# Optimization experiments

Measured on AMD Instinct MI355X. Metric: run time of the kernel, lower is better.

## Reference

```python
import jax, jax.numpy as jnp
import numpy as np

B, TK, N = 32, 2048, 1024  # batch, encoder steps, 2*hidden_dim


def setup_inputs() -> dict:
    key = jax.random.key(0)
    ks = jax.random.split(key, 12)
    s = 0.02
    return {
        "s_t_hat": jax.random.normal(ks[0], (B, N), jnp.float32),
        "h": jax.random.normal(ks[1], (B, TK, N), jnp.float32),
        "enc_padding_mask": jax.random.uniform(ks[2], (B, TK), jnp.float32),
        "coverage": jax.random.uniform(ks[3], (B, TK), jnp.float32),
        "q_h": jax.random.normal(ks[4], (B, TK, N), jnp.float32),
        "W_h": jax.random.normal(ks[5], (N, N), jnp.float32) * s,
        "W_q": jax.random.normal(ks[6], (N, N), jnp.float32) * s,
        "W_c": jax.random.normal(ks[7], (N,), jnp.float32) * s,   # Linear(1, N) weight, squeezed
        "W_d": jax.random.normal(ks[8], (N, N), jnp.float32) * s,  # decode_proj weight
        "b_d": jnp.zeros((N,), jnp.float32),                       # decode_proj bias
        "v_w": jax.random.normal(ks[9], (N,), jnp.float32) * s,    # v: Linear(N, 1) weight, squeezed
    }


def reference(s_t_hat, h, enc_padding_mask, coverage, q_h, W_h, W_q, W_c, W_d, b_d, v_w):
    # projections (Linear: y = x @ W.T)
    enc_feat = jnp.einsum("btn,mn->btm", h, W_h)            # [B,TK,N]
    q_feat = jnp.einsum("btn,mn->btm", q_h, W_q)            # [B,TK,N]
    dec_feat = s_t_hat @ W_d.T + b_d                         # [B,N]
    cov_feat = coverage[..., None] * W_c                     # [B,TK,N]
    att = jnp.tanh(enc_feat + dec_feat[:, None, :] + q_feat + cov_feat)
    scores = jnp.einsum("btn,n->bt", att, v_w)               # [B,TK]
    attn_ = jax.nn.softmax(scores, axis=1) * enc_padding_mask
    attn = attn_ / jnp.sum(attn_, axis=1, keepdims=True)     # renormalized
    c_t = jnp.einsum("bt,btn->bn", attn, h)                  # context vector
    coverage_out = coverage + attn
    return (c_t, attn, coverage_out)
```

## Files before the change

### kernel.cpp

```cpp
#include <hip/hip_runtime.h>
#include <stdint.h>

#define Bsz 32
#define TKs 2048
#define Nf  1024
#define Msz (Bsz*TKs)
#define KTOT 2048

typedef __bf16 bf16x8 __attribute__((ext_vector_type(8)));
typedef float  f32x4  __attribute__((ext_vector_type(4)));
typedef float  f32x16 __attribute__((ext_vector_type(16)));

__device__ __forceinline__ unsigned pack_bf2(float f0, float f1){
  unsigned u0 = __float_as_uint(f0) + 0x8000u;
  unsigned u1 = __float_as_uint(f1) + 0x8000u;
  return __builtin_amdgcn_perm(u1, u0, 0x07060302u);
}

__device__ __forceinline__ float fast_tanh(float x){
  float e = __expf(2.f * x);
  return 1.f - 2.f * __builtin_amdgcn_rcpf(e + 1.f);
}

__device__ __forceinline__ void async16(void* lds, const void* g){
  __builtin_amdgcn_global_load_lds(
      (const __attribute__((address_space(1))) unsigned int*)g,
      (__attribute__((address_space(3))) unsigned int*)lds,
      16, 0, 0);
}

__global__ __launch_bounds__(256) void pack_w_kernel(
    const float* __restrict__ Wh, const float* __restrict__ Wq,
    unsigned short* __restrict__ Wcat)
{
  int idx = (blockIdx.x * 256 + threadIdx.x) * 4;
  int m = idx >> 11;
  int k = idx & 2047;
  const float* src = (k < 1024) ? (Wh + m * 1024 + k) : (Wq + m * 1024 + (k - 1024));
  float4 v = *(const float4*)src;
  uint2 p;
  p.x = pack_bf2(v.x, v.y);
  p.y = pack_bf2(v.z, v.w);
  *(uint2*)(Wcat + idx) = p;
}

__global__ __launch_bounds__(256) void pack_a_kernel(
    const float* __restrict__ h, const float* __restrict__ q,
    unsigned short* __restrict__ Acat)
{
  size_t idx = ((size_t)blockIdx.x * 256 + threadIdx.x) * 8;
  size_t r = idx >> 11;
  int c = (int)(idx & 2047);
  const float* src = (c < 1024) ? (h + r * 1024 + c) : (q + r * 1024 + (c - 1024));
  float4 v0 = ((const float4*)src)[0];
  float4 v1 = ((const float4*)src)[1];
  uint4 p;
  p.x = pack_bf2(v0.x, v0.y); p.y = pack_bf2(v0.z, v0.w);
  p.z = pack_bf2(v1.x, v1.y); p.w = pack_bf2(v1.z, v1.w);
  *(uint4*)(Acat + idx) = p;
}

__global__ __launch_bounds__(256) void dec_kernel(
    const float* __restrict__ s_t, const float* __restrict__ Wd,
    const float* __restrict__ bd, float* __restrict__ dec)
{
  __shared__ float sv[1024];
  const int b = blockIdx.y;
  const int mbase = blockIdx.x * 64;
  for (int i = threadIdx.x; i < 1024; i += 256) sv[i] = s_t[b * 1024 + i];
  __syncthreads();
  const int wave = threadIdx.x >> 6, lane = threadIdx.x & 63;
  #pragma unroll 4
  for (int i = 0; i < 16; ++i){
    int m = mbase + wave * 16 + i;
    const float4* wr = (const float4*)(Wd + (size_t)m * 1024 + lane * 16);
    const float4* sr = (const float4*)(sv + lane * 16);
    float s = 0.f;
    #pragma unroll
    for (int j = 0; j < 4; ++j){
      float4 w = wr[j], x = sr[j];
      s += w.x * x.x + w.y * x.y + w.z * x.z + w.w * x.w;
    }
    #pragma unroll
    for (int d = 1; d < 64; d <<= 1) s += __shfl_xor(s, d);
    if (lane == 0) dec[b * 1024 + m] = s + bd[m];
  }
}

__global__ __launch_bounds__(256) void gemm_fused_fast(
    const unsigned short* __restrict__ Acat,
    const unsigned short* __restrict__ Wcat,
    const float* __restrict__ dec, const float* __restrict__ cov,
    const float* __restrict__ Wc, const float* __restrict__ vw,
    float* __restrict__ scoresP)
{
  __shared__ __align__(16) unsigned short As[128 * 32];
  __shared__ __align__(16) unsigned short Bs[128 * 32];
  __shared__ float ssum[2][128];
  __shared__ float covS[128];

  const int tid  = threadIdx.x;
  const int wave = tid >> 6, lane = tid & 63;
  const int wm = wave & 1, wn = wave >> 1;
  const int l31 = lane & 31, half = lane >> 5;

  const int p = blockIdx.x;
  const int ntile = (p >> 3) & 7;
  const int mtile = (p & 7) + ((p >> 6) << 3);
  const size_t growbase = (size_t)mtile * 128;

  if (tid < 128) covS[tid] = cov[growbase + tid];

  f32x16 acc[2][2];
  #pragma unroll
  for (int i = 0; i < 2; ++i)
    #pragma unroll
    for (int j = 0; j < 2; ++j)
      #pragma unroll
      for (int r = 0; r < 16; ++r) acc[i][j][r] = 0.f;

  const int s0 = wave * 128 + lane;
  const int s1 = s0 + 64;
  const int r0 = s0 >> 2, g0 = (s0 & 3) ^ ((r0 >> 1) & 3);
  const int r1 = s1 >> 2, g1 = (s1 & 3) ^ ((r1 >> 1) & 3);
  const unsigned short* pA0 = Acat + (size_t)(mtile * 128 + r0) * 2048 + g0 * 8;
  const unsigned short* pA1 = Acat + (size_t)(mtile * 128 + r1) * 2048 + g1 * 8;
  const unsigned short* pB0 = Wcat + (size_t)(ntile * 128 + r0) * 2048 + g0 * 8;
  const unsigned short* pB1 = Wcat + (size_t)(ntile * 128 + r1) * 2048 + g1 * 8;
  unsigned short* ldsA0 = &As[wave * 1024];
  unsigned short* ldsA1 = &As[wave * 1024 + 512];
  unsigned short* ldsB0 = &Bs[wave * 1024];
  unsigned short* ldsB1 = &Bs[wave * 1024 + 512];

  const bf16x8* a_rd[2][2];
  const bf16x8* b_rd[2][2];
  #pragma unroll
  for (int mi = 0; mi < 2; ++mi)
    #pragma unroll
    for (int ks = 0; ks < 2; ++ks){
      int row = wm * 64 + mi * 32 + l31;
      int g = ks * 2 + half;
      int pos = g ^ ((row >> 1) & 3);
      a_rd[mi][ks] = (const bf16x8*)&As[row * 32 + pos * 8];
    }
  #pragma unroll
  for (int ni = 0; ni < 2; ++ni)
    #pragma unroll
    for (int ks = 0; ks < 2; ++ks){
      int row = wn * 64 + ni * 32 + l31;
      int g = ks * 2 + half;
      int pos = g ^ ((row >> 1) & 3);
      b_rd[ni][ks] = (const bf16x8*)&Bs[row * 32 + pos * 8];
    }

  for (int kt = 0; kt < KTOT / 32; ++kt){
    async16(ldsA0, pA0);
    async16(ldsA1, pA1);
    async16(ldsB0, pB0);
    async16(ldsB1, pB1);
    pA0 += 32; pA1 += 32; pB0 += 32; pB1 += 32;
    __syncthreads();
    bf16x8 af[2][2], bg[2][2];
    #pragma unroll
    for (int i = 0; i < 2; ++i)
      #pragma unroll
      for (int ks = 0; ks < 2; ++ks){ af[i][ks] = *a_rd[i][ks]; bg[i][ks] = *b_rd[i][ks]; }
    #pragma unroll
    for (int ks = 0; ks < 2; ++ks)
      #pragma unroll
      for (int mi = 0; mi < 2; ++mi)
        #pragma unroll
        for (int ni = 0; ni < 2; ++ni)
          acc[mi][ni] = __builtin_amdgcn_mfma_f32_32x32x16_bf16(
              af[mi][ks], bg[ni][ks], acc[mi][ni], 0, 0, 0);
    __syncthreads();
  }

  const int brow = (mtile * 128) >> 11;
  const float* decb = dec + brow * 1024;
  float dv[2], wc2[2], vw2[2];
  #pragma unroll
  for (int ni = 0; ni < 2; ++ni){
    int col = ntile * 128 + wn * 64 + ni * 32 + l31;
    dv[ni]  = decb[col];
    wc2[ni] = Wc[col];
    vw2[ni] = vw[col];
  }
  #pragma unroll
  for (int mi = 0; mi < 2; ++mi){
    #pragma unroll
    for (int r = 0; r < 16; ++r){
      int rl = wm * 64 + mi * 32 + (r & 3) + 8 * (r >> 2) + 4 * half;
      float cv = covS[rl];
      float s = 0.f;
      #pragma unroll
      for (int ni = 0; ni < 2; ++ni){
        float x = acc[mi][ni][r] + dv[ni] + cv * wc2[ni];
        s += vw2[ni] * fast_tanh(x);
      }
      #pragma unroll
      for (int d = 1; d < 32; d <<= 1) s += __shfl_xor(s, d);
      if (l31 == 0) ssum[wn][rl] = s;
    }
  }
  __syncthreads();
  if (tid < 128)
    scoresP[(size_t)ntile * Msz + growbase + tid] = ssum[0][tid] + ssum[1][tid];
}

#define AST 40

__global__ __launch_bounds__(256) void gemm_fused_fb(
    const float* __restrict__ h, const float* __restrict__ q,
    const unsigned short* __restrict__ Wcat,
    const float* __restrict__ dec, const float* __restrict__ cov,
    const float* __restrict__ Wc, const float* __restrict__ vw,
    float* __restrict__ scoresP)
{
  __shared__ unsigned short As[128 * AST];
  __shared__ unsigned short Bs[128 * AST];
  __shared__ float ssum[2][128];

  const int tid  = threadIdx.x;
  const int wave = tid >> 6, lane = tid & 63;
  const int wm = wave & 1, wn = wave >> 1;
  const int quad = lane >> 4, low = lane & 15;
  const int ntile = blockIdx.x;
  const int mtile = blockIdx.y;

  f32x4 acc[4][4];
  #pragma unroll
  for (int i = 0; i < 4; ++i)
    #pragma unroll
    for (int j = 0; j < 4; ++j) acc[i][j] = (f32x4){0.f, 0.f, 0.f, 0.f};

  const int sr = tid >> 1;
  const int sh = (tid & 1) * 16;
  const size_t a_goff = ((size_t)(mtile * 128 + sr)) * 1024 + sh;
  const size_t b_goff = ((size_t)(ntile * 128 + sr)) * 2048 + sh;
  unsigned short* a_st = &As[sr * AST + sh];
  unsigned short* b_st = &Bs[sr * AST + sh];

  const bf16x8* a_rd[4];
  const bf16x8* b_rd[4];
  #pragma unroll
  for (int i = 0; i < 4; ++i){
    a_rd[i] = (const bf16x8*)&As[(wm * 64 + i * 16 + low) * AST + quad * 8];
    b_rd[i] = (const bf16x8*)&Bs[(wn * 64 + i * 16 + low) * AST + quad * 8];
  }

  for (int kt = 0; kt < KTOT / 32; ++kt){
    const int k0 = kt * 32;
    {
      const float* src = (k0 < 1024) ? (h + a_goff + k0) : (q + a_goff + (k0 - 1024));
      float4 v0 = ((const float4*)src)[0];
      float4 v1 = ((const float4*)src)[1];
      float4 v2 = ((const float4*)src)[2];
      float4 v3 = ((const float4*)src)[3];
      uint4 p0, p1;
      p0.x = pack_bf2(v0.x, v0.y); p0.y = pack_bf2(v0.z, v0.w);
      p0.z = pack_bf2(v1.x, v1.y); p0.w = pack_bf2(v1.z, v1.w);
      p1.x = pack_bf2(v2.x, v2.y); p1.y = pack_bf2(v2.z, v2.w);
      p1.z = pack_bf2(v3.x, v3.y); p1.w = pack_bf2(v3.z, v3.w);
      ((uint4*)a_st)[0] = p0;
      ((uint4*)a_st)[1] = p1;
    }
    {
      const uint4* src = (const uint4*)(Wcat + b_goff + k0);
      uint4 w0 = src[0];
      uint4 w1 = src[1];
      ((uint4*)b_st)[0] = w0;
      ((uint4*)b_st)[1] = w1;
    }
    __syncthreads();
    bf16x8 af[4], bg[4];
    #pragma unroll
    for (int i = 0; i < 4; ++i){ af[i] = *a_rd[i]; bg[i] = *b_rd[i]; }
    #pragma unroll
    for (int mi = 0; mi < 4; ++mi)
      #pragma unroll
      for (int ni = 0; ni < 4; ++ni)
        acc[mi][ni] = __builtin_amdgcn_mfma_f32_16x16x32_bf16(af[mi], bg[ni], acc[mi][ni], 0, 0, 0);
    __syncthreads();
  }

  const int brow = (mtile * 128) >> 11;
  const float* decb = dec + brow * 1024;
  const int colbase = ntile * 128 + wn * 64 + low;
  float dv[4], wc4[4], vw4[4];
  #pragma unroll
  for (int ni = 0; ni < 4; ++ni){
    int col = colbase + ni * 16;
    dv[ni]  = decb[col];
    wc4[ni] = Wc[col];
    vw4[ni] = vw[col];
  }
  const size_t growbase = (size_t)mtile * 128;
  const int rowloc0 = wm * 64 + quad * 4;
  #pragma unroll
  for (int mi = 0; mi < 4; ++mi){
    #pragma unroll
    for (int r = 0; r < 4; ++r){
      int rl = rowloc0 + mi * 16 + r;
      float cv = cov[growbase + rl];
      float s = 0.f;
      #pragma unroll
      for (int ni = 0; ni < 4; ++ni){
        float x = acc[mi][ni][r] + dv[ni] + cv * wc4[ni];
        s += vw4[ni] * fast_tanh(x);
      }
      #pragma unroll
      for (int d = 1; d < 16; d <<= 1) s += __shfl_xor(s, d);
      if (low == 0) ssum[wn][rl] = s;
    }
  }
  __syncthreads();
  if (tid < 128)
    scoresP[(size_t)ntile * Msz + growbase + tid] = ssum[0][tid] + ssum[1][tid];
}

__global__ __launch_bounds__(256) void softmax_kernel(
    const float* __restrict__ scoresP, const float* __restrict__ mask,
    const float* __restrict__ cov, float* __restrict__ attn_o,
    float* __restrict__ cov_o)
{
  const int b = blockIdx.x;
  const int tid = threadIdx.x;
  const int wave = tid >> 6, lane = tid & 63;
  __shared__ float redm[4], reds[4];
  float sc[8];
  float mx = -3.4e38f;
  #pragma unroll
  for (int j = 0; j < 8; ++j){
    int t = tid + j * 256;
    float s = 0.f;
    #pragma unroll
    for (int p = 0; p < 8; ++p) s += scoresP[(size_t)p * Msz + b * TKs + t];
    sc[j] = s;
    mx = fmaxf(mx, s);
  }
  #pragma unroll
  for (int d = 1; d < 64; d <<= 1) mx = fmaxf(mx, __shfl_xor(mx, d));
  if (lane == 0) redm[wave] = mx;
  __syncthreads();
  mx = fmaxf(fmaxf(redm[0], redm[1]), fmaxf(redm[2], redm[3]));
  float e[8]; float sum = 0.f;
  #pragma unroll
  for (int j = 0; j < 8; ++j){
    int t = tid + j * 256;
    float v = __expf(sc[j] - mx) * mask[b * TKs + t];
    e[j] = v; sum += v;
  }
  #pragma unroll
  for (int d = 1; d < 64; d <<= 1) sum += __shfl_xor(sum, d);
  if (lane == 0) reds[wave] = sum;
  __syncthreads();
  sum = reds[0] + reds[1] + reds[2] + reds[3];
  float inv = 1.f / sum;
  #pragma unroll
  for (int j = 0; j < 8; ++j){
    int t = tid + j * 256;
    float a = e[j] * inv;
    attn_o[b * TKs + t] = a;
    cov_o[b * TKs + t]  = cov[b * TKs + t] + a;
  }
}

__global__ __launch_bounds__(256) void ct_partial_bf(
    const unsigned short* __restrict__ Acat, const float* __restrict__ attn,
    float* __restrict__ P)
{
  const int b = blockIdx.y, tc = blockIdx.x;
  const int c4 = threadIdx.x * 4;
  float4 acc = {0.f, 0.f, 0.f, 0.f};
  const size_t rbase = (size_t)b * TKs + tc * 64;
  const float* ab = attn + b * TKs + tc * 64;
  #pragma unroll 4
  for (int tt = 0; tt < 64; ++tt){
    float a = ab[tt];
    uint2 v = *(const uint2*)(Acat + (rbase + tt) * 2048 + c4);
    acc.x += a * __uint_as_float(v.x << 16);
    acc.y += a * __uint_as_float(v.x & 0xffff0000u);
    acc.z += a * __uint_as_float(v.y << 16);
    acc.w += a * __uint_as_float(v.y & 0xffff0000u);
  }
  *(float4*)(P + ((size_t)(tc * Bsz + b)) * Nf + c4) = acc;
}

__global__ __launch_bounds__(256) void ct_partial(
    const float* __restrict__ h, const float* __restrict__ attn,
    float* __restrict__ P)
{
  const int b = blockIdx.y, tc = blockIdx.x;
  const int n4 = threadIdx.x * 4;
  float4 acc = {0.f, 0.f, 0.f, 0.f};
  const float* hb = h + ((size_t)b * TKs + tc * 64) * Nf;
  const float* ab = attn + b * TKs + tc * 64;
  #pragma unroll 4
  for (int tt = 0; tt < 64; ++tt){
    float a = ab[tt];
    float4 hv = *(const float4*)(hb + (size_t)tt * Nf + n4);
    acc.x += a * hv.x; acc.y += a * hv.y; acc.z += a * hv.z; acc.w += a * hv.w;
  }
  *(float4*)(P + ((size_t)(tc * Bsz + b)) * Nf + n4) = acc;
}

__global__ __launch_bounds__(256) void ct_reduce(
    const float* __restrict__ P, float* __restrict__ out)
{
  int bn = (blockIdx.x * 256 + threadIdx.x) * 4;
  float4 s = {0.f, 0.f, 0.f, 0.f};
  for (int j = 0; j < 32; ++j){
    float4 v = *(const float4*)(P + (size_t)j * (Bsz * Nf) + bn);
    s.x += v.x; s.y += v.y; s.z += v.z; s.w += v.w;
  }
  *(float4*)(out + bn) = s;
}

extern "C" void kernel_launch(void* const* d_in, const int* in_sizes, int n_in,
                              void* d_out, int out_size, void* d_ws, size_t ws_size,
                              hipStream_t stream) {
  const float* s_t  = (const float*)d_in[0];
  const float* h    = (const float*)d_in[1];
  const float* mask = (const float*)d_in[2];
  const float* cov  = (const float*)d_in[3];
  const float* qh   = (const float*)d_in[4];
  const float* Wh   = (const float*)d_in[5];
  const float* Wq   = (const float*)d_in[6];
  const float* Wc   = (const float*)d_in[7];
  const float* Wd   = (const float*)d_in[8];
  const float* bd   = (const float*)d_in[9];
  const float* vw   = (const float*)d_in[10];

  float* out    = (float*)d_out;
  float* c_t    = out;
  float* attn_o = out + Bsz * Nf;
  float* cov_o  = attn_o + Bsz * TKs;

  char* ws = (char*)d_ws;
  unsigned short* Wcat = (unsigned short*)ws;
  float* dec     = (float*)(ws + (4u << 20));
  float* scoresP = (float*)(ws + (4u << 20) + (128u << 10));
  float* ctP     = (float*)(ws + (6u << 20) + (128u << 10));
  unsigned short* Acat = (unsigned short*)(ws + (16ull << 20));

  const size_t need_fast = (16ull << 20) + (size_t)Msz * KTOT * 2;
  const bool fast = (ws_size >= need_fast);

  hipLaunchKernelGGL(pack_w_kernel, dim3(2048), dim3(256), 0, stream, Wh, Wq, Wcat);
  hipLaunchKernelGGL(dec_kernel,    dim3(16, 32), dim3(256), 0, stream, s_t, Wd, bd, dec);
  if (fast){
    hipLaunchKernelGGL(pack_a_kernel, dim3((unsigned)((size_t)Msz * KTOT / 8 / 256)),
                       dim3(256), 0, stream, h, qh, Acat);
    hipLaunchKernelGGL(gemm_fused_fast, dim3(4096), dim3(256), 0, stream,
                       Acat, Wcat, dec, cov, Wc, vw, scoresP);
  } else {
    hipLaunchKernelGGL(gemm_fused_fb, dim3(8, 512), dim3(256), 0, stream,
                       h, qh, Wcat, dec, cov, Wc, vw, scoresP);
  }
  hipLaunchKernelGGL(softmax_kernel, dim3(32), dim3(256), 0, stream,
                     scoresP, mask, cov, attn_o, cov_o);
  if (fast){
    hipLaunchKernelGGL(ct_partial_bf, dim3(32, 32), dim3(256), 0, stream, Acat, attn_o, ctP);
  } else {
    hipLaunchKernelGGL(ct_partial, dim3(32, 32), dim3(256), 0, stream, h, attn_o, ctP);
  }
  hipLaunchKernelGGL(ct_reduce,  dim3(32), dim3(256), 0, stream, ctP, c_t);
}
```

Baseline: 964.5 us.

## Fuse fp32-to-bf16 A conversion into GEMM loop, drop separate pack pass

Removes the pack_a kernel and the large bf16 Acat workspace; the GEMM now loads fp32 h/q rows directly, converts them to bf16 in registers and stores into LDS, with a register prefetch of the next k-tile. The context-vector pass now reads fp32 h instead of the bf16 copy, and the fallback GEMM path is deleted. This saves a full write and read of the packed activation tensor at the cost of more global A traffic per GEMM tile and synchronous loads instead of async LDS copies.

```diff
diff --git a/kernel.cpp b/kernel.cpp
--- a/kernel.cpp
+++ b/kernel.cpp
@@ -42,22 +42,6 @@
   p.x = pack_bf2(v.x, v.y);
   p.y = pack_bf2(v.z, v.w);
   *(uint2*)(Wcat + idx) = p;
-}
-
-__global__ __launch_bounds__(256) void pack_a_kernel(
-    const float* __restrict__ h, const float* __restrict__ q,
-    unsigned short* __restrict__ Acat)
-{
-  size_t idx = ((size_t)blockIdx.x * 256 + threadIdx.x) * 8;
-  size_t r = idx >> 11;
-  int c = (int)(idx & 2047);
-  const float* src = (c < 1024) ? (h + r * 1024 + c) : (q + r * 1024 + (c - 1024));
-  float4 v0 = ((const float4*)src)[0];
-  float4 v1 = ((const float4*)src)[1];
-  uint4 p;
-  p.x = pack_bf2(v0.x, v0.y); p.y = pack_bf2(v0.z, v0.w);
-  p.z = pack_bf2(v1.x, v1.y); p.w = pack_bf2(v1.z, v1.w);
-  *(uint4*)(Acat + idx) = p;
 }
 
 __global__ __launch_bounds__(256) void dec_kernel(
@@ -88,7 +72,7 @@
 }
 
 __global__ __launch_bounds__(256) void gemm_fused_fast(
-    const unsigned short* __restrict__ Acat,
+    const float* __restrict__ h, const float* __restrict__ q,
     const unsigned short* __restrict__ Wcat,
     const float* __restrict__ dec, const float* __restrict__ cov,
     const float* __restrict__ Wc, const float* __restrict__ vw,
@@ -123,12 +107,14 @@
   const int s1 = s0 + 64;
   const int r0 = s0 >> 2, g0 = (s0 & 3) ^ ((r0 >> 1) & 3);
   const int r1 = s1 >> 2, g1 = (s1 & 3) ^ ((r1 >> 1) & 3);
-  const unsigned short* pA0 = Acat + (size_t)(mtile * 128 + r0) * 2048 + g0 * 8;
-  const unsigned short* pA1 = Acat + (size_t)(mtile * 128 + r1) * 2048 + g1 * 8;
+
+  const size_t aOff0 = (size_t)(mtile * 128 + r0) * 1024 + g0 * 8;
+  const size_t aOff1 = (size_t)(mtile * 128 + r1) * 1024 + g1 * 8;
+  unsigned short* stA0 = &As[s0 * 8];
+  unsigned short* stA1 = &As[s1 * 8];
+
   const unsigned short* pB0 = Wcat + (size_t)(ntile * 128 + r0) * 2048 + g0 * 8;
   const unsigned short* pB1 = Wcat + (size_t)(ntile * 128 + r1) * 2048 + g1 * 8;
-  unsigned short* ldsA0 = &As[wave * 1024];
-  unsigned short* ldsA1 = &As[wave * 1024 + 512];
   unsigned short* ldsB0 = &Bs[wave * 1024];
   unsigned short* ldsB1 = &Bs[wave * 1024 + 512];
 
@@ -153,13 +139,33 @@
       b_rd[ni][ks] = (const bf16x8*)&Bs[row * 32 + pos * 8];
     }
 
+  float4 pf00 = *(const float4*)(h + aOff0);
+  float4 pf01 = *(const float4*)(h + aOff0 + 4);
+  float4 pf10 = *(const float4*)(h + aOff1);
+  float4 pf11 = *(const float4*)(h + aOff1 + 4);
+
   for (int kt = 0; kt < KTOT / 32; ++kt){
-    async16(ldsA0, pA0);
-    async16(ldsA1, pA1);
+    uint4 w0, w1;
+    w0.x = pack_bf2(pf00.x, pf00.y); w0.y = pack_bf2(pf00.z, pf00.w);
+    w0.z = pack_bf2(pf01.x, pf01.y); w0.w = pack_bf2(pf01.z, pf01.w);
+    w1.x = pack_bf2(pf10.x, pf10.y); w1.y = pack_bf2(pf10.z, pf10.w);
+    w1.z = pack_bf2(pf11.x, pf11.y); w1.w = pack_bf2(pf11.z, pf11.w);
+    *(uint4*)stA0 = w0;
+    *(uint4*)stA1 = w1;
     async16(ldsB0, pB0);
     async16(ldsB1, pB1);
-    pA0 += 32; pA1 += 32; pB0 += 32; pB1 += 32;
+    pB0 += 32; pB1 += 32;
     __syncthreads();
+
+    if (kt < KTOT / 32 - 1){
+      int c = ((kt + 1) * 32) & 1023;
+      const float* sp = (kt + 1 < 32) ? h : q;
+      pf00 = *(const float4*)(sp + aOff0 + c);
+      pf01 = *(const float4*)(sp + aOff0 + c + 4);
+      pf10 = *(const float4*)(sp + aOff1 + c);
+      pf11 = *(const float4*)(sp + aOff1 + c + 4);
+    }
+
     bf16x8 af[2][2], bg[2][2];
     #pragma unroll
     for (int i = 0; i < 2; ++i)
@@ -208,117 +214,6 @@
     scoresP[(size_t)ntile * Msz + growbase + tid] = ssum[0][tid] + ssum[1][tid];
 }
 
-#define AST 40
-
-__global__ __launch_bounds__(256) void gemm_fused_fb(
-    const float* __restrict__ h, const float* __restrict__ q,
-    const unsigned short* __restrict__ Wcat,
-    const float* __restrict__ dec, const float* __restrict__ cov,
-    const float* __restrict__ Wc, const float* __restrict__ vw,
-    float* __restrict__ scoresP)
-{
-  __shared__ unsigned short As[128 * AST];
-  __shared__ unsigned short Bs[128 * AST];
-  __shared__ float ssum[2][128];
-
-  const int tid  = threadIdx.x;
-  const int wave = tid >> 6, lane = tid & 63;
-  const int wm = wave & 1, wn = wave >> 1;
-  const int quad = lane >> 4, low = lane & 15;
-  const int ntile = blockIdx.x;
-  const int mtile = blockIdx.y;
-
-  f32x4 acc[4][4];
-  #pragma unroll
-  for (int i = 0; i < 4; ++i)
-    #pragma unroll
-    for (int j = 0; j < 4; ++j) acc[i][j] = (f32x4){0.f, 0.f, 0.f, 0.f};
-
-  const int sr = tid >> 1;
-  const int sh = (tid & 1) * 16;
-  const size_t a_goff = ((size_t)(mtile * 128 + sr)) * 1024 + sh;
-  const size_t b_goff = ((size_t)(ntile * 128 + sr)) * 2048 + sh;
-  unsigned short* a_st = &As[sr * AST + sh];
-  unsigned short* b_st = &Bs[sr * AST + sh];
-
-  const bf16x8* a_rd[4];
-  const bf16x8* b_rd[4];
-  #pragma unroll
-  for (int i = 0; i < 4; ++i){
-    a_rd[i] = (const bf16x8*)&As[(wm * 64 + i * 16 + low) * AST + quad * 8];
-    b_rd[i] = (const bf16x8*)&Bs[(wn * 64 + i * 16 + low) * AST + quad * 8];
-  }
-
-  for (int kt = 0; kt < KTOT / 32; ++kt){
-    const int k0 = kt * 32;
-    {
-      const float* src = (k0 < 1024) ? (h + a_goff + k0) : (q + a_goff + (k0 - 1024));
-      float4 v0 = ((const float4*)src)[0];
-      float4 v1 = ((const float4*)src)[1];
-      float4 v2 = ((const float4*)src)[2];
-      float4 v3 = ((const float4*)src)[3];
-      uint4 p0, p1;
-      p0.x = pack_bf2(v0.x, v0.y); p0.y = pack_bf2(v0.z, v0.w);
-      p0.z = pack_bf2(v1.x, v1.y); p0.w = pack_bf2(v1.z, v1.w);
-      p1.x = pack_bf2(v2.x, v2.y); p1.y = pack_bf2(v2.z, v2.w);
-      p1.z = pack_bf2(v3.x, v3.y); p1.w = pack_bf2(v3.z, v3.w);
-      ((uint4*)a_st)[0] = p0;
-      ((uint4*)a_st)[1] = p1;
-    }
-    {
-      const uint4* src = (const uint4*)(Wcat + b_goff + k0);
-      uint4 w0 = src[0];
-      uint4 w1 = src[1];
-      ((uint4*)b_st)[0] = w0;
-      ((uint4*)b_st)[1] = w1;
-    }
-    __syncthreads();
-    bf16x8 af[4], bg[4];
-    #pragma unroll
-    for (int i = 0; i < 4; ++i){ af[i] = *a_rd[i]; bg[i] = *b_rd[i]; }
-    #pragma unroll
-    for (int mi = 0; mi < 4; ++mi)
-      #pragma unroll
-      for (int ni = 0; ni < 4; ++ni)
-        acc[mi][ni] = __builtin_amdgcn_mfma_f32_16x16x32_bf16(af[mi], bg[ni], acc[mi][ni], 0, 0, 0);
-    __syncthreads();
-  }
-
-  const int brow = (mtile * 128) >> 11;
-  const float* decb = dec + brow * 1024;
-  const int colbase = ntile * 128 + wn * 64 + low;
-  float dv[4], wc4[4], vw4[4];
-  #pragma unroll
-  for (int ni = 0; ni < 4; ++ni){
-    int col = colbase + ni * 16;
-    dv[ni]  = decb[col];
-    wc4[ni] = Wc[col];
-    vw4[ni] = vw[col];
-  }
-  const size_t growbase = (size_t)mtile * 128;
-  const int rowloc0 = wm * 64 + quad * 4;
-  #pragma unroll
-  for (int mi = 0; mi < 4; ++mi){
-    #pragma unroll
-    for (int r = 0; r < 4; ++r){
-      int rl = rowloc0 + mi * 16 + r;
-      float cv = cov[growbase + rl];
-      float s = 0.f;
-      #pragma unroll
-      for (int ni = 0; ni < 4; ++ni){
-        float x = acc[mi][ni][r] + dv[ni] + cv * wc4[ni];
-        s += vw4[ni] * fast_tanh(x);
-      }
-      #pragma unroll
-      for (int d = 1; d < 16; d <<= 1) s += __shfl_xor(s, d);
-      if (low == 0) ssum[wn][rl] = s;
-    }
-  }
-  __syncthreads();
-  if (tid < 128)
-    scoresP[(size_t)ntile * Msz + growbase + tid] = ssum[0][tid] + ssum[1][tid];
-}
-
 __global__ __launch_bounds__(256) void softmax_kernel(
     const float* __restrict__ scoresP, const float* __restrict__ mask,
     const float* __restrict__ cov, float* __restrict__ attn_o,
@@ -364,27 +259,6 @@
     attn_o[b * TKs + t] = a;
     cov_o[b * TKs + t]  = cov[b * TKs + t] + a;
   }
-}
-
-__global__ __launch_bounds__(256) void ct_partial_bf(
-    const unsigned short* __restrict__ Acat, const float* __restrict__ attn,
-    float* __restrict__ P)
-{
-  const int b = blockIdx.y, tc = blockIdx.x;
-  const int c4 = threadIdx.x * 4;
-  float4 acc = {0.f, 0.f, 0.f, 0.f};
-  const size_t rbase = (size_t)b * TKs + tc * 64;
-  const float* ab = attn + b * TKs + tc * 64;
-  #pragma unroll 4
-  for (int tt = 0; tt < 64; ++tt){
-    float a = ab[tt];
-    uint2 v = *(const uint2*)(Acat + (rbase + tt) * 2048 + c4);
-    acc.x += a * __uint_as_float(v.x << 16);
-    acc.y += a * __uint_as_float(v.x & 0xffff0000u);
-    acc.z += a * __uint_as_float(v.y << 16);
-    acc.w += a * __uint_as_float(v.y & 0xffff0000u);
-  }
-  *(float4*)(P + ((size_t)(tc * Bsz + b)) * Nf + c4) = acc;
 }
 
 __global__ __launch_bounds__(256) void ct_partial(
@@ -442,28 +316,13 @@
   float* dec     = (float*)(ws + (4u << 20));
   float* scoresP = (float*)(ws + (4u << 20) + (128u << 10));
   float* ctP     = (float*)(ws + (6u << 20) + (128u << 10));
-  unsigned short* Acat = (unsigned short*)(ws + (16ull << 20));
-
-  const size_t need_fast = (16ull << 20) + (size_t)Msz * KTOT * 2;
-  const bool fast = (ws_size >= need_fast);
 
   hipLaunchKernelGGL(pack_w_kernel, dim3(2048), dim3(256), 0, stream, Wh, Wq, Wcat);
   hipLaunchKernelGGL(dec_kernel,    dim3(16, 32), dim3(256), 0, stream, s_t, Wd, bd, dec);
-  if (fast){
-    hipLaunchKernelGGL(pack_a_kernel, dim3((unsigned)((size_t)Msz * KTOT / 8 / 256)),
-                       dim3(256), 0, stream, h, qh, Acat);
-    hipLaunchKernelGGL(gemm_fused_fast, dim3(4096), dim3(256), 0, stream,
-                       Acat, Wcat, dec, cov, Wc, vw, scoresP);
-  } else {
-    hipLaunchKernelGGL(gemm_fused_fb, dim3(8, 512), dim3(256), 0, stream,
-                       h, qh, Wcat, dec, cov, Wc, vw, scoresP);
-  }
+  hipLaunchKernelGGL(gemm_fused_fast, dim3(4096), dim3(256), 0, stream,
+                     h, qh, Wcat, dec, cov, Wc, vw, scoresP);
   hipLaunchKernelGGL(softmax_kernel, dim3(32), dim3(256), 0, stream,
                      scoresP, mask, cov, attn_o, cov_o);
-  if (fast){
-    hipLaunchKernelGGL(ct_partial_bf, dim3(32, 32), dim3(256), 0, stream, Acat, attn_o, ctP);
-  } else {
-    hipLaunchKernelGGL(ct_partial, dim3(32, 32), dim3(256), 0, stream, h, attn_o, ctP);
-  }
+  hipLaunchKernelGGL(ct_partial, dim3(32, 32), dim3(256), 0, stream, h, attn_o, ctP);
   hipLaunchKernelGGL(ct_reduce,  dim3(32), dim3(256), 0, stream, ctP, c_t);
 }
```

After: 996.2 us. 3.3% more time.
